# Performance work log

Hardware: AMD Instinct MI355X
Metric: run time of the kernel (lower is better)

Reference implementation:

```python
import jax, jax.numpy as jnp
import numpy as np

B, NP, N, C, H = 16, 512, 1024, 1024, 16
HD = C // H
HID = 4 * C
EPS = 1e-5


def _layernorm(x, g, b):
    mu = jnp.mean(x, axis=-1, keepdims=True)
    var = jnp.mean(jnp.square(x - mu), axis=-1, keepdims=True)
    return (x - mu) * jax.lax.rsqrt(var + EPS) * g + b


def setup_inputs() -> dict:
    key = jax.random.key(0)
    ks = jax.random.split(key, 12)
    x = jax.random.normal(ks[0], (B, NP, C), dtype=jnp.float32)
    cache_k = jax.random.normal(ks[1], (B, H, N, HD), dtype=jnp.float32)
    cache_v = jax.random.normal(ks[2], (B, H, N, HD), dtype=jnp.float32)
    # update_mask: exactly NP active (to-be-updated) token slots per batch row
    scores = jax.random.uniform(ks[3], (B, N))
    top = jnp.argsort(scores, axis=1)[:, :NP]
    update_mask = jnp.zeros((B, N), dtype=bool).at[jnp.arange(B)[:, None], top].set(True)
    s = 0.02
    qkv_w = jax.random.normal(ks[4], (C, 3 * C), dtype=jnp.float32) * s
    qkv_b = jnp.zeros((3 * C,), dtype=jnp.float32)
    proj_w = jax.random.normal(ks[5], (C, C), dtype=jnp.float32) * s
    proj_b = jnp.zeros((C,), dtype=jnp.float32)
    n1_g = jnp.ones((C,), dtype=jnp.float32)
    n1_b = jnp.zeros((C,), dtype=jnp.float32)
    n2_g = jnp.ones((C,), dtype=jnp.float32)
    n2_b = jnp.zeros((C,), dtype=jnp.float32)
    fc1_w = jax.random.normal(ks[6], (C, HID), dtype=jnp.float32) * s
    fc1_b = jnp.zeros((HID,), dtype=jnp.float32)
    fc2_w = jax.random.normal(ks[7], (HID, C), dtype=jnp.float32) * s
    fc2_b = jnp.zeros((C,), dtype=jnp.float32)
    return dict(x=x, cache_k=cache_k, cache_v=cache_v, update_mask=update_mask,
                qkv_w=qkv_w, qkv_b=qkv_b, proj_w=proj_w, proj_b=proj_b,
                n1_g=n1_g, n1_b=n1_b, n2_g=n2_g, n2_b=n2_b,
                fc1_w=fc1_w, fc1_b=fc1_b, fc2_w=fc2_w, fc2_b=fc2_b)


def reference(x, cache_k, cache_v, update_mask, qkv_w, qkv_b, proj_w, proj_b,
              n1_g, n1_b, n2_g, n2_b, fc1_w, fc1_b, fc2_w, fc2_b):
    Bq, Np, Cd = x.shape
    h = _layernorm(x, n1_g, n1_b)
    qkv = (h @ qkv_w + qkv_b).reshape(Bq, Np, 3, H, HD)
    q, k, v = jnp.moveaxis(qkv, 2, 0)               # each [B, Np, H, HD]
    q = jnp.swapaxes(q, 1, 2)                       # [B, H, Np, HD]
    k = jnp.swapaxes(k, 1, 2)
    v = jnp.swapaxes(v, 1, 2)
    # masked_scatter_: i-th new token -> i-th masked slot (row-uniform mask count)
    idx = jnp.argsort(jnp.logical_not(update_mask), axis=1)[:, :Np]  # [B, Np]
    k_full = jax.vmap(lambda c, i, kn: c.at[:, i, :].set(kn))(cache_k, idx, k)
    v_full = jax.vmap(lambda c, i, vn: c.at[:, i, :].set(vn))(cache_v, idx, v)
    scale = HD ** -0.5
    attn = jnp.einsum('bhqd,bhkd->bhqk', q * scale, k_full)  # [B,H,Np,N]
    attn = jax.nn.softmax(attn, axis=-1)
    o = jnp.einsum('bhqk,bhkd->bhqd', attn, v_full)
    o = jnp.swapaxes(o, 1, 2).reshape(Bq, Np, Cd)
    o = o @ proj_w + proj_b
    x = x + o
    h2 = _layernorm(x, n2_g, n2_b)
    mlp = jax.nn.gelu(h2 @ fc1_w + fc1_b, approximate=False) @ fc2_w + fc2_b
    return x + mlp
```

## Files before the change

kernel.cpp:

```cpp
#include <hip/hip_runtime.h>
#include <hip/hip_bf16.h>
#include <math.h>

#define Bd   16
#define NPd  512
#define Nd   1024
#define Cd   1024
#define Hd   16
#define HDd  64
#define HIDd 4096
#define EPSd 1e-5f

typedef unsigned short u16;
typedef __bf16 bf16x8 __attribute__((ext_vector_type(8)));
typedef float  f32x4  __attribute__((ext_vector_type(4)));

__device__ __forceinline__ u16 f2bf(float f) {
    unsigned int u = __builtin_bit_cast(unsigned int, f);
    u = u + 0x7fffu + ((u >> 16) & 1u);
    return (u16)(u >> 16);
}

__device__ __forceinline__ void async_load16(const void* g, void* l) {
    __builtin_amdgcn_global_load_lds(
        (const __attribute__((address_space(1))) void*)(uintptr_t)g,
        (__attribute__((address_space(3))) void*)(unsigned int)(uintptr_t)l,
        16, 0, 0);
}

__global__ __launch_bounds__(256) void build_src(const void* __restrict__ mask_raw,
                                                 int* __restrict__ src) {
    const int b = blockIdx.x;
    const int t = threadIdx.x;
    const unsigned char* m8 = (const unsigned char*)mask_raw;
    const int* m32 = (const int*)mask_raw;

    int c = 0;
    #pragma unroll
    for (int i = 0; i < 4; i++) c += (m8[b * Nd + t * 4 + i] != 0) ? 1 : 0;
    #pragma unroll
    for (int off = 1; off < 64; off <<= 1) c += __shfl_xor(c, off);
    __shared__ int warr[4];
    if ((t & 63) == 0) warr[t >> 6] = c;
    __syncthreads();
    const int c8 = warr[0] + warr[1] + warr[2] + warr[3];
    const bool use8 = (c8 == NPd);

    int f[4];
    #pragma unroll
    for (int i = 0; i < 4; i++) {
        const int n = t * 4 + i;
        f[i] = use8 ? (m8[b * Nd + n] != 0) : (m32[b * Nd + n] != 0);
    }
    const int loc = f[0] + f[1] + f[2] + f[3];

    int sc_ = loc;
    #pragma unroll
    for (int off = 1; off < 64; off <<= 1) {
        const int u = __shfl_up(sc_, off);
        if ((t & 63) >= off) sc_ += u;
    }
    __shared__ int wtot[4];
    __syncthreads();
    if ((t & 63) == 63) wtot[t >> 6] = sc_;
    __syncthreads();
    int base = 0;
    for (int w = 0; w < (t >> 6); w++) base += wtot[w];

    int run = base + sc_ - loc;
    #pragma unroll
    for (int i = 0; i < 4; i++) {
        const int n = t * 4 + i;
        src[b * Nd + n] = f[i] ? run : -1;
        run += f[i];
    }
}

__global__ __launch_bounds__(256) void ln_kernel(const float* __restrict__ x,
                                                 const float* __restrict__ g,
                                                 const float* __restrict__ bb,
                                                 u16* __restrict__ out) {
    const int row = blockIdx.x;
    const int t = threadIdx.x;
    const float* xr = x + (size_t)row * Cd;
    const float4 v = *(const float4*)(xr + t * 4);
    float s = v.x + v.y + v.z + v.w;
    float q = v.x * v.x + v.y * v.y + v.z * v.z + v.w * v.w;
    #pragma unroll
    for (int off = 1; off < 64; off <<= 1) {
        s += __shfl_xor(s, off);
        q += __shfl_xor(q, off);
    }
    __shared__ float ss[4], qq[4];
    if ((t & 63) == 0) { ss[t >> 6] = s; qq[t >> 6] = q; }
    __syncthreads();
    s = ss[0] + ss[1] + ss[2] + ss[3];
    q = qq[0] + qq[1] + qq[2] + qq[3];
    const float mu = s * (1.0f / Cd);
    const float var = q * (1.0f / Cd) - mu * mu;
    const float rs = rsqrtf(var + EPSd);
    const float4 gv = *(const float4*)(g + t * 4);
    const float4 bv = *(const float4*)(bb + t * 4);
    ushort4 r;
    r.x = f2bf((v.x - mu) * rs * gv.x + bv.x);
    r.y = f2bf((v.y - mu) * rs * gv.y + bv.y);
    r.z = f2bf((v.z - mu) * rs * gv.z + bv.z);
    r.w = f2bf((v.w - mu) * rs * gv.w + bv.w);
    *(ushort4*)(out + (size_t)row * Cd + t * 4) = r;
}

__global__ __launch_bounds__(256) void conv_t(const float* __restrict__ W,
                                              u16* __restrict__ Wt,
                                              int K, int N) {
    __shared__ float tile[32][33];
    const int k0 = blockIdx.y * 32;
    const int n0 = blockIdx.x * 32;
    const int t = threadIdx.x;
    const int row = t >> 3, c4 = (t & 7) * 4;
    const float4 v = *(const float4*)(W + (size_t)(k0 + row) * N + n0 + c4);
    tile[row][c4 + 0] = v.x;
    tile[row][c4 + 1] = v.y;
    tile[row][c4 + 2] = v.z;
    tile[row][c4 + 3] = v.w;
    __syncthreads();
    ushort4 o;
    o.x = f2bf(tile[c4 + 0][row]);
    o.y = f2bf(tile[c4 + 1][row]);
    o.z = f2bf(tile[c4 + 2][row]);
    o.w = f2bf(tile[c4 + 3][row]);
    *(ushort4*)(Wt + (size_t)(n0 + row) * K + k0 + c4) = o;
}

template <int EPI, typename OUT_T>
__global__ __launch_bounds__(256) void gemm_mfma(const u16* __restrict__ A,
                                                 const u16* __restrict__ Wt,
                                                 const float* __restrict__ bias,
                                                 const float* __restrict__ res,
                                                 OUT_T* __restrict__ out,
                                                 int K, int Nn) {
    __shared__ u16 As[128 * 32];
    __shared__ u16 Bs[128 * 32];

    const int t = threadIdx.x;
    const int L = t & 63;
    const int w = t >> 6;
    const int wm = w >> 1, wn = w & 1;
    const int m0 = blockIdx.y * 128;
    const int n0 = blockIdx.x * 128;

    const int srow = 32 * w + (L >> 2);
    const int scol = (L & 3) * 8;
    const u16* ap0 = A  + (size_t)(m0 + srow) * K + scol;
    const u16* ap1 = ap0 + (size_t)16 * K;
    const u16* bp0 = Wt + (size_t)(n0 + srow) * K + scol;
    const u16* bp1 = bp0 + (size_t)16 * K;
    u16* alds0 = As + w * 1024;
    u16* alds1 = alds0 + 512;
    u16* blds0 = Bs + w * 1024;
    u16* blds1 = blds0 + 512;

    f32x4 acc[4][4];
    const f32x4 zero = {0.f, 0.f, 0.f, 0.f};
    #pragma unroll
    for (int i = 0; i < 4; i++)
        #pragma unroll
        for (int j = 0; j < 4; j++) acc[i][j] = zero;

    const int frag_off = (L & 15) * 32 + (L >> 4) * 8;

    for (int kt = 0; kt < K; kt += 32) {
        __syncthreads();
        async_load16(ap0 + kt, alds0);
        async_load16(ap1 + kt, alds1);
        async_load16(bp0 + kt, blds0);
        async_load16(bp1 + kt, blds1);
        __syncthreads();

        bf16x8 a[4], b[4];
        #pragma unroll
        for (int i = 0; i < 4; i++) {
            a[i] = *(const bf16x8*)&As[(wm * 64 + i * 16) * 32 + frag_off];
            b[i] = *(const bf16x8*)&Bs[(wn * 64 + i * 16) * 32 + frag_off];
        }
        #pragma unroll
        for (int i = 0; i < 4; i++)
            #pragma unroll
            for (int j = 0; j < 4; j++)
                acc[i][j] = __builtin_amdgcn_mfma_f32_16x16x32_bf16(a[i], b[j], acc[i][j], 0, 0, 0);
    }

    const int cn = n0 + wn * 64 + (L & 15);
    const int cm = m0 + wm * 64 + (L >> 4) * 4;
    #pragma unroll
    for (int i = 0; i < 4; i++) {
        #pragma unroll
        for (int j = 0; j < 4; j++) {
            const int nn = cn + j * 16;
            const float bv = bias[nn];
            #pragma unroll
            for (int r = 0; r < 4; r++) {
                const int mm = cm + i * 16 + r;
                float v = acc[i][j][r] + bv;
                if (EPI == 2) v = 0.5f * v * (1.0f + erff(v * 0.70710678118654752f));
                if (EPI == 1) v += res[(size_t)mm * Nn + nn];
                if constexpr (sizeof(OUT_T) == 2) out[(size_t)mm * Nn + nn] = (OUT_T)f2bf(v);
                else out[(size_t)mm * Nn + nn] = v;
            }
        }
    }
}

__global__ __launch_bounds__(256) void kv_cast(const u16* __restrict__ qkv,
                                               const float* __restrict__ ck,
                                               const float* __restrict__ cv,
                                               const int* __restrict__ srcArr,
                                               u16* __restrict__ Kb,
                                               u16* __restrict__ Vtb) {
    const int id = blockIdx.x;
    const int nt = id & 15, hh = (id >> 4) & 15, b = id >> 8;
    const int t = threadIdx.x;
    __shared__ u16 Vl[64][72];

    const int row = t >> 2;
    const int dd = (t & 3) * 16;
    const int n = nt * 64 + row;
    const int sidx = srcArr[b * Nd + n];

    u16 kv16[16], vv16[16];
    if (sidx >= 0) {
        const u16* kp = qkv + (size_t)(b * NPd + sidx) * 3072 + Cd + hh * 64 + dd;
        const u16* vp = kp + Cd;
        *(ulonglong2*)&kv16[0] = *(const ulonglong2*)kp;
        *(ulonglong2*)&kv16[8] = *(const ulonglong2*)(kp + 8);
        *(ulonglong2*)&vv16[0] = *(const ulonglong2*)vp;
        *(ulonglong2*)&vv16[8] = *(const ulonglong2*)(vp + 8);
    } else {
        const float* kp = ck + ((size_t)((b * Hd + hh) * Nd + n)) * HDd + dd;
        const float* vp = cv + ((size_t)((b * Hd + hh) * Nd + n)) * HDd + dd;
        #pragma unroll
        for (int c = 0; c < 4; c++) {
            const float4 kc4 = *(const float4*)(kp + c * 4);
            const float4 vc4 = *(const float4*)(vp + c * 4);
            kv16[c * 4 + 0] = f2bf(kc4.x); kv16[c * 4 + 1] = f2bf(kc4.y);
            kv16[c * 4 + 2] = f2bf(kc4.z); kv16[c * 4 + 3] = f2bf(kc4.w);
            vv16[c * 4 + 0] = f2bf(vc4.x); vv16[c * 4 + 1] = f2bf(vc4.y);
            vv16[c * 4 + 2] = f2bf(vc4.z); vv16[c * 4 + 3] = f2bf(vc4.w);
        }
    }

    u16* ko = Kb + ((size_t)((b * Hd + hh) * Nd + n)) * HDd + dd;
    *(ulonglong2*)ko = *(ulonglong2*)&kv16[0];
    *(ulonglong2*)(ko + 8) = *(ulonglong2*)&kv16[8];

    #pragma unroll
    for (int i = 0; i < 16; i++) Vl[row][dd + i] = vv16[i];
    __syncthreads();

    const int d = t >> 2, nc = (t & 3) * 16;
    u16 ov[16];
    #pragma unroll
    for (int i = 0; i < 16; i++) ov[i] = Vl[nc + i][d];
    u16* vo = Vtb + ((size_t)((b * Hd + hh) * HDd + d)) * Nd + nt * 64 + nc;
    *(ulonglong2*)vo = *(ulonglong2*)&ov[0];
    *(ulonglong2*)(vo + 8) = *(ulonglong2*)&ov[8];
}

__global__ __launch_bounds__(256) void attn_mfma(const u16* __restrict__ qkv,
                                                 const u16* __restrict__ Kb,
                                                 const u16* __restrict__ Vtb,
                                                 u16* __restrict__ attno) {
    const int bh = blockIdx.x;
    const int qt = blockIdx.y;
    const int b = bh >> 4, hh = bh & 15;
    const int t = threadIdx.x;
    const int L = t & 63;
    const int w = t >> 6;

    __shared__ u16 Qs[4096];
    __shared__ u16 Ks[4096];
    __shared__ u16 Vs[4096];
    __shared__ u16 Ps[4][16 * 72];

    const size_t kbase = (size_t)((b * Hd + hh) * Nd) * HDd;
    const size_t vbase = (size_t)((b * Hd + hh) * HDd) * Nd;

    #pragma unroll
    for (int j = 0; j < 2; j++) {
        const int row = 16 * w + 8 * j + (L >> 3);
        const int ch = (L & 7) ^ (row & 7);
        const u16* g = qkv + (size_t)(b * NPd + qt * 64 + row) * 3072 + hh * 64 + ch * 8;
        async_load16(g, Qs + (16 * w + 8 * j) * 64);
    }

    f32x4 acc[4];
    const f32x4 zero = {0.f, 0.f, 0.f, 0.f};
    #pragma unroll
    for (int nb = 0; nb < 4; nb++) acc[nb] = zero;
    float m_run[4] = {-INFINITY, -INFINITY, -INFINITY, -INFINITY};
    float l_run[4] = {0.f, 0.f, 0.f, 0.f};

    for (int kt = 0; kt < 16; kt++) {
        __syncthreads();
        #pragma unroll
        for (int j = 0; j < 2; j++) {
            const int row = 16 * w + 8 * j + (L >> 3);
            const int ch = (L & 7) ^ (row & 7);
            async_load16(Kb + kbase + (size_t)(kt * 64 + row) * 64 + ch * 8,
                         Ks + (16 * w + 8 * j) * 64);
            async_load16(Vtb + vbase + (size_t)row * Nd + kt * 64 + ch * 8,
                         Vs + (16 * w + 8 * j) * 64);
        }
        __syncthreads();

        const int qrow = 16 * w + (L & 15);
        const bf16x8 aq0 = *(const bf16x8*)&Qs[qrow * 64 + (((L >> 4)     ^ (L & 7)) * 8)];
        const bf16x8 aq1 = *(const bf16x8*)&Qs[qrow * 64 + (((4 + (L >> 4)) ^ (L & 7)) * 8)];

        f32x4 s[4];
        #pragma unroll
        for (int kb = 0; kb < 4; kb++) {
            const int krow = kb * 16 + (L & 15);
            const bf16x8 bk0 = *(const bf16x8*)&Ks[krow * 64 + (((L >> 4)     ^ (L & 7)) * 8)];
            const bf16x8 bk1 = *(const bf16x8*)&Ks[krow * 64 + (((4 + (L >> 4)) ^ (L & 7)) * 8)];
            s[kb] = __builtin_amdgcn_mfma_f32_16x16x32_bf16(aq0, bk0, zero, 0, 0, 0);
            s[kb] = __builtin_amdgcn_mfma_f32_16x16x32_bf16(aq1, bk1, s[kb], 0, 0, 0);
        }

        float al[4];
        float pb[4][4];
        #pragma unroll
        for (int r = 0; r < 4; r++) {
            float m = fmaxf(fmaxf(s[0][r], s[1][r]), fmaxf(s[2][r], s[3][r])) * 0.125f;
            m = fmaxf(m, __shfl_xor(m, 1));
            m = fmaxf(m, __shfl_xor(m, 2));
            m = fmaxf(m, __shfl_xor(m, 4));
            m = fmaxf(m, __shfl_xor(m, 8));
            const float mn = fmaxf(m_run[r], m);
            al[r] = __expf(m_run[r] - mn);
            m_run[r] = mn;
        }
        float ps[4] = {0.f, 0.f, 0.f, 0.f};
        #pragma unroll
        for (int kb = 0; kb < 4; kb++)
            #pragma unroll
            for (int r = 0; r < 4; r++) {
                const float p = __expf(s[kb][r] * 0.125f - m_run[r]);
                pb[kb][r] = p;
                ps[r] += p;
            }
        #pragma unroll
        for (int r = 0; r < 4; r++) {
            ps[r] += __shfl_xor(ps[r], 1);
            ps[r] += __shfl_xor(ps[r], 2);
            ps[r] += __shfl_xor(ps[r], 4);
            ps[r] += __shfl_xor(ps[r], 8);
            l_run[r] = l_run[r] * al[r] + ps[r];
        }
        #pragma unroll
        for (int nb = 0; nb < 4; nb++)
            #pragma unroll
            for (int r = 0; r < 4; r++) acc[nb][r] *= al[r];

        u16* pw = &Ps[w][0];
        #pragma unroll
        for (int kb = 0; kb < 4; kb++)
            #pragma unroll
            for (int r = 0; r < 4; r++)
                pw[((L >> 4) * 4 + r) * 72 + kb * 16 + (L & 15)] = f2bf(pb[kb][r]);

        const bf16x8 ap0 = *(const bf16x8*)&Ps[w][(L & 15) * 72 +      (L >> 4) * 8];
        const bf16x8 ap1 = *(const bf16x8*)&Ps[w][(L & 15) * 72 + 32 + (L >> 4) * 8];
        #pragma unroll
        for (int nb = 0; nb < 4; nb++) {
            const int drow = nb * 16 + (L & 15);
            const bf16x8 bv0 = *(const bf16x8*)&Vs[drow * 64 + (((L >> 4)     ^ (L & 7)) * 8)];
            const bf16x8 bv1 = *(const bf16x8*)&Vs[drow * 64 + (((4 + (L >> 4)) ^ (L & 7)) * 8)];
            acc[nb] = __builtin_amdgcn_mfma_f32_16x16x32_bf16(ap0, bv0, acc[nb], 0, 0, 0);
            acc[nb] = __builtin_amdgcn_mfma_f32_16x16x32_bf16(ap1, bv1, acc[nb], 0, 0, 0);
        }
    }

    float inv[4];
    #pragma unroll
    for (int r = 0; r < 4; r++) inv[r] = 1.0f / l_run[r];
    #pragma unroll
    for (int nb = 0; nb < 4; nb++)
        #pragma unroll
        for (int r = 0; r < 4; r++) {
            const int q = qt * 64 + w * 16 + (L >> 4) * 4 + r;
            const int d = nb * 16 + (L & 15);
            attno[(size_t)(b * NPd + q) * Cd + hh * 64 + d] = f2bf(acc[nb][r] * inv[r]);
        }
}

extern "C" void kernel_launch(void* const* d_in, const int* in_sizes, int n_in,
                              void* d_out, int out_size, void* d_ws, size_t ws_size,
                              hipStream_t stream) {
    const float* x       = (const float*)d_in[0];
    const float* cache_k = (const float*)d_in[1];
    const float* cache_v = (const float*)d_in[2];
    const void*  mask    = d_in[3];
    const float* qkv_w   = (const float*)d_in[4];
    const float* qkv_b   = (const float*)d_in[5];
    const float* proj_w  = (const float*)d_in[6];
    const float* proj_b  = (const float*)d_in[7];
    const float* n1_g    = (const float*)d_in[8];
    const float* n1_b    = (const float*)d_in[9];
    const float* n2_g    = (const float*)d_in[10];
    const float* n2_b    = (const float*)d_in[11];
    const float* fc1_w   = (const float*)d_in[12];
    const float* fc1_b   = (const float*)d_in[13];
    const float* fc2_w   = (const float*)d_in[14];
    const float* fc2_b   = (const float*)d_in[15];
    float* out = (float*)d_out;

    const size_t MR = (size_t)Bd * NPd;
    char* ws = (char*)d_ws;
    int*   srcArr = (int*)ws;
    float* x2     = (float*)(ws + 65536);
    u16*   h      = (u16*)(x2 + MR * Cd);
    u16*   attno  = h + MR * Cd;
    u16*   qkv    = attno + MR * Cd;
    u16*   Kb     = qkv + MR * 3 * Cd;
    u16*   Vtb    = Kb + (size_t)Bd * Hd * Nd * HDd;
    u16*   m1     = qkv;
    u16*   qkv_wt = Vtb + (size_t)Bd * Hd * Nd * HDd;
    u16*   proj_wt= qkv_wt + (size_t)3 * Cd * Cd;
    u16*   fc1_wt = proj_wt + (size_t)Cd * Cd;
    u16*   fc2_wt = fc1_wt + (size_t)Cd * HIDd;

    build_src<<<Bd, 256, 0, stream>>>(mask, srcArr);
    conv_t<<<dim3(3 * Cd / 32, Cd / 32),  256, 0, stream>>>(qkv_w,  qkv_wt,  Cd,   3 * Cd);
    conv_t<<<dim3(Cd / 32, Cd / 32),      256, 0, stream>>>(proj_w, proj_wt, Cd,   Cd);
    conv_t<<<dim3(HIDd / 32, Cd / 32),    256, 0, stream>>>(fc1_w,  fc1_wt,  Cd,   HIDd);
    conv_t<<<dim3(Cd / 32, HIDd / 32),    256, 0, stream>>>(fc2_w,  fc2_wt,  HIDd, Cd);

    ln_kernel<<<MR, 256, 0, stream>>>(x, n1_g, n1_b, h);
    gemm_mfma<0, u16><<<dim3(3 * Cd / 128, MR / 128), 256, 0, stream>>>(h, qkv_wt, qkv_b, nullptr, qkv, Cd, 3 * Cd);
    kv_cast<<<Bd * Hd * (Nd / 64), 256, 0, stream>>>(qkv, cache_k, cache_v, srcArr, Kb, Vtb);
    attn_mfma<<<dim3(Bd * Hd, NPd / 64), 256, 0, stream>>>(qkv, Kb, Vtb, attno);
    gemm_mfma<1, float><<<dim3(Cd / 128, MR / 128), 256, 0, stream>>>(attno, proj_wt, proj_b, x, x2, Cd, Cd);
    ln_kernel<<<MR, 256, 0, stream>>>(x2, n2_g, n2_b, h);
    gemm_mfma<2, u16><<<dim3(HIDd / 128, MR / 128), 256, 0, stream>>>(h, fc1_wt, fc1_b, nullptr, m1, Cd, HIDd);
    gemm_mfma<1, float><<<dim3(Cd / 128, MR / 128), 256, 0, stream>>>(m1, fc2_wt, fc2_b, x2, out, HIDd, Cd);
}
```

Baseline: 700.2 us.

## Double-buffer GEMM LDS tiles and remap blocks across XCDs for GEMM and attention

The GEMM main loop now keeps two LDS buffers for the A and B tiles. It issues the async global-to-LDS loads for the next K-step before running the MFMAs on the current one, so each iteration needs one barrier instead of two and the loads overlap with compute. Block IDs in both the GEMM and attention kernels are remapped so that consecutive logical tiles land on the same XCD, which should improve L2 reuse of shared weight and KV data. The cost is twice the LDS per GEMM block, which may reduce occupancy, and the remap assumes the block count divides evenly by 8.

Measured after the change: 681.1 us. 1.03x faster.

```diff
diff --git a/kernel.cpp b/kernel.cpp
--- a/kernel.cpp
+++ b/kernel.cpp
@@ -10,6 +10,7 @@
 #define HDd  64
 #define HIDd 4096
 #define EPSd 1e-5f
+#define MRd  (Bd * NPd)
 
 typedef unsigned short u16;
 typedef __bf16 bf16x8 __attribute__((ext_vector_type(8)));
@@ -138,15 +139,20 @@
                                                  const float* __restrict__ res,
                                                  OUT_T* __restrict__ out,
                                                  int K, int Nn) {
-    __shared__ u16 As[128 * 32];
-    __shared__ u16 Bs[128 * 32];
+    __shared__ u16 As[2][128 * 32];
+    __shared__ u16 Bs[2][128 * 32];
 
     const int t = threadIdx.x;
     const int L = t & 63;
     const int w = t >> 6;
     const int wm = w >> 1, wn = w & 1;
-    const int m0 = blockIdx.y * 128;
-    const int n0 = blockIdx.x * 128;
+
+    const int gx = gridDim.x;
+    const int nwg = gx * gridDim.y;
+    int id = blockIdx.y * gx + blockIdx.x;
+    id = (id & 7) * (nwg >> 3) + (id >> 3);
+    const int m0 = (id / gx) * 128;
+    const int n0 = (id % gx) * 128;
 
     const int srow = 32 * w + (L >> 2);
     const int scol = (L & 3) * 8;
@@ -154,10 +160,6 @@
     const u16* ap1 = ap0 + (size_t)16 * K;
     const u16* bp0 = Wt + (size_t)(n0 + srow) * K + scol;
     const u16* bp1 = bp0 + (size_t)16 * K;
-    u16* alds0 = As + w * 1024;
-    u16* alds1 = alds0 + 512;
-    u16* blds0 = Bs + w * 1024;
-    u16* blds1 = blds0 + 512;
 
     f32x4 acc[4][4];
     const f32x4 zero = {0.f, 0.f, 0.f, 0.f};
@@ -167,26 +169,39 @@
         for (int j = 0; j < 4; j++) acc[i][j] = zero;
 
     const int frag_off = (L & 15) * 32 + (L >> 4) * 8;
-
-    for (int kt = 0; kt < K; kt += 32) {
-        __syncthreads();
-        async_load16(ap0 + kt, alds0);
-        async_load16(ap1 + kt, alds1);
-        async_load16(bp0 + kt, blds0);
-        async_load16(bp1 + kt, blds1);
-        __syncthreads();
+    const int nsteps = K >> 5;
+
+    async_load16(ap0, &As[0][w * 1024]);
+    async_load16(ap1, &As[0][w * 1024 + 512]);
+    async_load16(bp0, &Bs[0][w * 1024]);
+    async_load16(bp1, &Bs[0][w * 1024 + 512]);
+    __syncthreads();
+
+    int cur = 0;
+    for (int kt = 0; kt < nsteps; kt++) {
+        const int nxt = cur ^ 1;
+        if (kt + 1 < nsteps) {
+            const int off = (kt + 1) << 5;
+            async_load16(ap0 + off, &As[nxt][w * 1024]);
+            async_load16(ap1 + off, &As[nxt][w * 1024 + 512]);
+            async_load16(bp0 + off, &Bs[nxt][w * 1024]);
+            async_load16(bp1 + off, &Bs[nxt][w * 1024 + 512]);
+        }
 
         bf16x8 a[4], b[4];
         #pragma unroll
         for (int i = 0; i < 4; i++) {
-            a[i] = *(const bf16x8*)&As[(wm * 64 + i * 16) * 32 + frag_off];
-            b[i] = *(const bf16x8*)&Bs[(wn * 64 + i * 16) * 32 + frag_off];
+            a[i] = *(const bf16x8*)&As[cur][(wm * 64 + i * 16) * 32 + frag_off];
+            b[i] = *(const bf16x8*)&Bs[cur][(wn * 64 + i * 16) * 32 + frag_off];
         }
         #pragma unroll
         for (int i = 0; i < 4; i++)
             #pragma unroll
             for (int j = 0; j < 4; j++)
                 acc[i][j] = __builtin_amdgcn_mfma_f32_16x16x32_bf16(a[i], b[j], acc[i][j], 0, 0, 0);
+
+        __syncthreads();
+        cur = nxt;
     }
 
     const int cn = n0 + wn * 64 + (L & 15);
@@ -269,8 +284,10 @@
                                                  const u16* __restrict__ Kb,
                                                  const u16* __restrict__ Vtb,
                                                  u16* __restrict__ attno) {
-    const int bh = blockIdx.x;
-    const int qt = blockIdx.y;
+    const int orig = blockIdx.y * 256 + blockIdx.x;
+    const int xc = orig & 7, pos = orig >> 3;
+    const int bh = (xc << 5) | (pos >> 3);
+    const int qt = pos & 7;
     const int b = bh >> 4, hh = bh & 15;
     const int t = threadIdx.x;
     const int L = t & 63;
@@ -436,11 +453,15 @@
     conv_t<<<dim3(Cd / 32, HIDd / 32),    256, 0, stream>>>(fc2_w,  fc2_wt,  HIDd, Cd);
 
     ln_kernel<<<MR, 256, 0, stream>>>(x, n1_g, n1_b, h);
-    gemm_mfma<0, u16><<<dim3(3 * Cd / 128, MR / 128), 256, 0, stream>>>(h, qkv_wt, qkv_b, nullptr, qkv, Cd, 3 * Cd);
+    gemm_mfma<0, u16><<<dim3(3 * Cd / 128, MR / 128), 256, 0, stream>>>(
+        h, qkv_wt, qkv_b, nullptr, qkv, Cd, 3 * Cd);
     kv_cast<<<Bd * Hd * (Nd / 64), 256, 0, stream>>>(qkv, cache_k, cache_v, srcArr, Kb, Vtb);
     attn_mfma<<<dim3(Bd * Hd, NPd / 64), 256, 0, stream>>>(qkv, Kb, Vtb, attno);
-    gemm_mfma<1, float><<<dim3(Cd / 128, MR / 128), 256, 0, stream>>>(attno, proj_wt, proj_b, x, x2, Cd, Cd);
+    gemm_mfma<1, float><<<dim3(Cd / 128, MR / 128), 256, 0, stream>>>(
+        attno, proj_wt, proj_b, x, x2, Cd, Cd);
     ln_kernel<<<MR, 256, 0, stream>>>(x2, n2_g, n2_b, h);
-    gemm_mfma<2, u16><<<dim3(HIDd / 128, MR / 128), 256, 0, stream>>>(h, fc1_wt, fc1_b, nullptr, m1, Cd, HIDd);
-    gemm_mfma<1, float><<<dim3(Cd / 128, MR / 128), 256, 0, stream>>>(m1, fc2_wt, fc2_b, x2, out, HIDd, Cd);
-}
+    gemm_mfma<2, u16><<<dim3(HIDd / 128, MR / 128), 256, 0, stream>>>(
+        h, fc1_wt, fc1_b, nullptr, m1, Cd, HIDd);
+    gemm_mfma<1, float><<<dim3(Cd / 128, MR / 128), 256, 0, stream>>>(
+        m1, fc2_wt, fc2_b, x2, out, HIDd, Cd);
+}
```
